# Optimization experiments

Hardware: AMD Instinct MI355X
Metric: run time of the kernel (lower is better)

Reference implementation:

```python
import jax, jax.numpy as jnp
import numpy as np
from jax import lax

B, T, H, F, K, M, NB = 32, 1024, 256, 256, 3, 4096, 256


def setup_inputs() -> dict:
    key = jax.random.key(0)
    ks = jax.random.split(key, 10)
    s = 0.05
    inp = {}
    inp["x"] = jax.random.normal(ks[0], (B, T, H), jnp.float32)
    inp["src_mask"] = jnp.zeros((B, T), bool)
    inp["duration_target"] = jax.random.randint(ks[1], (B, T), 0, 7)
    inp["pitch_target"] = jax.random.uniform(ks[2], (B, T), jnp.float32)
    inp["energy_target"] = jax.random.uniform(ks[3], (B, T), jnp.float32)
    inp["max_len"] = M
    # stacked params for 3 predictors: [duration, pitch, energy]
    inp["w1"] = jax.random.normal(ks[4], (3, K, H, F), jnp.float32) * s  # WIO layout
    inp["b1"] = jnp.zeros((3, F), jnp.float32)
    inp["g1"] = jnp.ones((3, F), jnp.float32)
    inp["be1"] = jnp.zeros((3, F), jnp.float32)
    inp["w2"] = jax.random.normal(ks[5], (3, K, F, F), jnp.float32) * s
    inp["b2"] = jnp.zeros((3, F), jnp.float32)
    inp["g2"] = jnp.ones((3, F), jnp.float32)
    inp["be2"] = jnp.zeros((3, F), jnp.float32)
    inp["lw"] = jax.random.normal(ks[6], (3, F, 1), jnp.float32) * s
    inp["lb"] = jnp.zeros((3, 1), jnp.float32)
    inp["pitch_bins"] = jnp.linspace(0.0, 1.0, NB - 1, dtype=jnp.float32)
    inp["pitch_emb"] = jax.random.normal(ks[7], (NB, H), jnp.float32) * 0.1
    inp["energy_bins"] = jnp.linspace(0.0, 1.0, NB - 1, dtype=jnp.float32)
    inp["energy_emb"] = jax.random.normal(ks[8], (NB, H), jnp.float32) * 0.1
    return inp


def _conv_relu_ln(x, w, b, g, be):
    # Conv1d (k=3, pad=1) over seq dim with channels-last, then ReLU, then LayerNorm.
    h = lax.conv_general_dilated(x, w, (1,), [(1, 1)],
                                 dimension_numbers=('NWC', 'WIO', 'NWC'))
    h = jax.nn.relu(h + b)
    mu = jnp.mean(h, -1, keepdims=True)
    var = jnp.var(h, -1, keepdims=True)
    return (h - mu) * lax.rsqrt(var + 1e-5) * g + be


def _predictor(x, i, w1, b1, g1, be1, w2, b2, g2, be2, lw, lb, mask):
    h = _conv_relu_ln(x, w1[i], b1[i], g1[i], be1[i])
    h = _conv_relu_ln(h, w2[i], b2[i], g2[i], be2[i])
    out = (h @ lw[i] + lb[i])[..., 0]  # [B, T]
    return jnp.where(mask, 0.0, out)


def _length_regulate(x, dur, max_len):
    # vectorized version of the per-sample repeat/cat/pad LengthRegulator
    cum = jnp.cumsum(dur, axis=1)                     # [B, T]
    mel_len = jnp.minimum(cum[:, -1], max_len)        # [B]
    frames = jnp.arange(max_len)                      # [M]
    # frame j maps to phoneme i with cum[i-1] <= j < cum[i]
    idx = jax.vmap(lambda c: jnp.searchsorted(c, frames, side='right'))(cum)
    idx = jnp.minimum(idx, x.shape[1] - 1)
    out = jnp.take_along_axis(x, idx[:, :, None], axis=1)  # [B, M, H]
    valid = frames[None, :] < mel_len[:, None]
    return out * valid[:, :, None].astype(x.dtype), mel_len, ~valid


def reference(x, src_mask, duration_target, pitch_target, energy_target, max_len,
              w1, b1, g1, be1, w2, b2, g2, be2, lw, lb,
              pitch_bins, pitch_emb, energy_bins, energy_emb):
    P = (w1, b1, g1, be1, w2, b2, g2, be2, lw, lb)
    # predictor_grad = 1.0 -> x.detach() + 1.0*(x - x.detach()) == x
    log_dur = _predictor(x, 0, *P, src_mask)
    pitch_pred = _predictor(x, 1, *P, src_mask)
    p_e = pitch_emb[jnp.searchsorted(pitch_bins, pitch_target, side='left')]
    energy_pred = _predictor(x, 2, *P, src_mask)
    e_e = energy_emb[jnp.searchsorted(energy_bins, energy_target, side='left')]
    output = x + p_e + e_e
    out, mel_len, mel_mask = _length_regulate(output, duration_target, max_len)
    return (out, pitch_pred, energy_pred, log_dur, duration_target, mel_len, mel_mask)
```

## Files before the change

### kernel.cpp

```cpp
#include <hip/hip_runtime.h>
#include <hip/hip_bf16.h>
#include <stdint.h>


typedef __bf16 bf16;
typedef __attribute__((ext_vector_type(8))) __bf16 bf16x8;
typedef __attribute__((ext_vector_type(4))) float f32x4;

#define TSEQ 1024

#define O1 33554432
#define O2 33587200
#define O3 33619968
#define O4 33652736
#define O5 33685504
#define O6 33685536

#define OUT_END_B 135266432

#define XB_OFF 512
#define H1B_OFF (XB_OFF + 16777216)
#define H1B_SZ 16777216
#define WT_OFF (H1B_OFF + 3 * H1B_SZ)
#define WT_SZ 393216

#define XB_SZ 16777216
#define H1B_TOT (3 * H1B_SZ)
#define WT_TOT (6 * WT_SZ)
#define SCRATCH_SZ (XB_SZ + H1B_TOT + WT_TOT)

#define CUM_OFF 0
#define ADDROW_OFF 131072
#define ZEROS_OFF 262144
#define WS_SCR_OFF 524288
#define WS_NEED (WS_SCR_OFF + SCRATCH_SZ)

__global__ __launch_bounds__(256) void k_prep(
    const float* __restrict__ x, bf16* __restrict__ xb,
    const float* __restrict__ w1, const float* __restrict__ w2,
    bf16* __restrict__ wt,
    const float* __restrict__ pt, const float* __restrict__ et,
    const float* __restrict__ pbins, const float* __restrict__ ebins,
    int* __restrict__ addrow, float* __restrict__ zpage,
    const int* __restrict__ dur, const int* __restrict__ maxlen,
    float* __restrict__ out, int* __restrict__ cum) {
  int bid = blockIdx.x;
  int tid = threadIdx.x;
  if (bid < 4096) {
    int t = bid * 256 + tid;
    int g = t >> 5;
    int u = t & 31;
    const float4* s = (const float4*)(x + ((size_t)g << 8) + (u << 3));
    float4 a = s[0], b = s[1];
    bf16x8 o;
    o[0] = (bf16)a.x; o[1] = (bf16)a.y; o[2] = (bf16)a.z; o[3] = (bf16)a.w;
    o[4] = (bf16)b.x; o[5] = (bf16)b.y; o[6] = (bf16)b.z; o[7] = (bf16)b.w;
    *(bf16x8*)(xb + ((size_t)g << 8) + (u << 3)) = o;
  } else if (bid < 4672) {
    int bw = bid - 4096;
    int m = bw / 96;
    int r = bw % 96;
    int f = (r & 3) * 64 + (tid & 63);
    int u = (r >> 2) * 4 + (tid >> 6);
    const float* W = (m < 3) ? w1 : w2;
    int i = (m < 3) ? m : m - 3;
    int dt = u >> 5;
    int c0 = (u & 31) << 3;
    const float* src = W + (((size_t)(i * 3 + dt) * 256 + c0) << 8) + f;
    bf16x8 o;
#pragma unroll
    for (int cc = 0; cc < 8; ++cc) o[cc] = (bf16)src[(size_t)cc << 8];
    *(bf16x8*)(wt + (size_t)m * 196608 + (size_t)f * 768 + (u << 3)) = o;
  } else if (bid < 4800) {
    __shared__ float pb[255], eb[255];
    if (tid < 255) { pb[tid] = pbins[tid]; eb[tid] = ebins[tid]; }
    if (bid == 4672 && tid < 64) zpage[tid] = 0.f;
    __syncthreads();
    int g = (bid - 4672) * 256 + tid;
    float pv = pt[g], ev = et[g];
    int lo = 0, hi = 255;
    while (lo < hi) { int md = (lo + hi) >> 1; if (pb[md] < pv) lo = md + 1; else hi = md; }
    int pi = lo;
    lo = 0; hi = 255;
    while (lo < hi) { int md = (lo + hi) >> 1; if (eb[md] < ev) lo = md + 1; else hi = md; }
    addrow[g] = pi | (lo << 16);
  } else {
    __shared__ int lds[256];
    int b = bid - 4800;
    int4 d = ((const int4*)(dur + b * 1024))[tid];
    int p0 = d.x, p1 = p0 + d.y, p2 = p1 + d.z, p3 = p2 + d.w;
    int val = p3;
    lds[tid] = val;
    __syncthreads();
    for (int off = 1; off < 256; off <<= 1) {
      int t = (tid >= off) ? lds[tid - off] : 0;
      __syncthreads();
      val += t;
      lds[tid] = val;
      __syncthreads();
    }
    int excl = val - p3;
    int4 c;
    c.x = excl + p0; c.y = excl + p1; c.z = excl + p2; c.w = excl + p3;
    ((int4*)(cum + b * 1024))[tid] = c;
    float4 fd;
    fd.x = (float)d.x; fd.y = (float)d.y; fd.z = (float)d.z; fd.w = (float)d.w;
    ((float4*)(out + O4 + b * 1024))[tid] = fd;
    if (tid == 255) {
      int mel = val < maxlen[0] ? val : maxlen[0];
      out[O5 + b] = (float)mel;
    }
  }
}

__global__ __launch_bounds__(256, 2) void k_conv(
    const char* __restrict__ Ab, size_t AperY, const char* __restrict__ Wb,
    const float* __restrict__ bias0, const float* __restrict__ gamma0,
    const float* __restrict__ beta0, char* __restrict__ hout0,
    const float* __restrict__ lw0, const float* __restrict__ lb0,
    const unsigned char* __restrict__ mask, float* __restrict__ outb,
    const char* __restrict__ zpage, int mode,
    const float* __restrict__ xf, const int* __restrict__ cum,
    const int* __restrict__ addrow, const float* __restrict__ pemb,
    const float* __restrict__ eemb, const int* __restrict__ maxlen,
    int lrbase) {
  __shared__ __align__(16) char Abuf[2][8192];
  __shared__ __align__(16) char Bbuf[2][16384];
  __shared__ float redS[128][2];
  __shared__ float redS2[128][2];
  __shared__ float predr[128][2];

  const int tid = threadIdx.x;
  const int bid = blockIdx.x;

  if (bid >= 768) {
    int* cl = (int*)Abuf;
    int rid0 = lrbase + ((bid - 768) << 4);
    int b = rid0 >> 12;
    ((int4*)cl)[tid] = ((const int4*)(cum + (b << 10)))[tid];
    __syncthreads();
    int lane = tid & 63;
    int wv = tid >> 6;
    int total = cl[1023];
    int ml = maxlen[0];
    int mel = total < ml ? total : ml;
    int c1 = cl[lane * 16 + 15];
#pragma unroll
    for (int rr = 0; rr < 4; ++rr) {
      int rid = rid0 + (wv << 2) + rr;
      int j = rid & 4095;
      bool valid = j < mel;
      float4 res = {0.f, 0.f, 0.f, 0.f};
      if (valid) {
        unsigned long long m1 = __ballot(j < c1);
        int s = __ffsll(m1) - 1;
        unsigned long long m2 = __ballot(j < cl[s * 16 + (lane & 15)]);
        int p = __ffsll(m2) - 1;
        int i = s * 16 + p;
        int ar = addrow[(b << 10) + i];
        int pi = ar & 0xffff, ei = ar >> 16;
        const float4* xr = (const float4*)(xf + (((size_t)(b << 10) + i) << 8));
        const float4* pr = (const float4*)(pemb + ((size_t)pi << 8));
        const float4* er = (const float4*)(eemb + ((size_t)ei << 8));
        float4 a = xr[lane], pp = pr[lane], e = er[lane];
        res.x = a.x + pp.x + e.x;
        res.y = a.y + pp.y + e.y;
        res.z = a.z + pp.z + e.z;
        res.w = a.w + pp.w + e.w;
      }
      ((float4*)(outb + ((size_t)rid << 8)))[lane] = res;
      if (lane == 0) outb[O6 + rid] = valid ? 0.f : 1.f;
    }
    return;
  }

  const int wv = tid >> 6;
  const int ln = tid & 63;
  const int q = ln >> 4;
  const int m16 = ln & 15;
  const int rh = wv >> 1;
  const int ch = wv & 1;
  const int y = bid >> 8;
  const int g0 = (bid & 255) << 7;
  const int t0 = g0 & (TSEQ - 1);

  const char* A = Ab + (size_t)y * AperY;
  const char* W = Wb + (size_t)y * WT_SZ;

  const int srow = ln >> 2;
  const int slot = ln & 3;
  const int usw = slot ^ ((ln >> 3) & 3);

  const char* bsrc[4];
#pragma unroll
  for (int j = 0; j < 4; ++j) {
    int f = j * 64 + wv * 16 + srow;
    bsrc[j] = W + ((size_t)f * 768 + usw * 8) * 2;
  }
  const int rbase = wv * 16 + srow;

  f32x4 acc[4][8];
#pragma unroll
  for (int a = 0; a < 4; a++)
#pragma unroll
    for (int b = 0; b < 8; b++) acc[a][b] = (f32x4){0.f, 0.f, 0.f, 0.f};

#define STAGE(KB, BUF)                                                         \
  {                                                                            \
    int dt0_ = (KB) >> 3;                                                      \
    int c0_ = ((KB) & 7) << 5;                                                 \
    _Pragma("unroll") for (int j = 0; j < 2; ++j) {                            \
      int rr = j * 64 + rbase + dt0_ - 1;                                      \
      const char* src = ((unsigned)(t0 + rr) < 1024u)                          \
          ? A + (((size_t)(g0 + rr) << 8) + c0_ + usw * 8) * 2                 \
          : zpage + slot * 16;                                                 \
      __builtin_amdgcn_global_load_lds(                                        \
          (const __attribute__((address_space(1))) void*)src,                  \
          (__attribute__((address_space(3))) void*)(Abuf[BUF] + j * 4096 +     \
                                                    tid * 16),                 \
          16, 0, 0);                                                           \
    }                                                                          \
    _Pragma("unroll") for (int j = 0; j < 4; ++j) {                            \
      __builtin_amdgcn_global_load_lds(                                        \
          (const __attribute__((address_space(1))) void*)(bsrc[j] + (KB)*64),  \
          (__attribute__((address_space(3))) void*)(Bbuf[BUF] + j * 4096 +     \
                                                    tid * 16),                 \
          16, 0, 0);                                                           \
    }                                                                          \
  }

  const int spq = (q ^ ((m16 >> 1) & 3)) << 4;
  const int aoff = (rh * 64 + m16) * 64 + spq;
  const int boff = (ch * 128 + m16) * 64 + spq;

  STAGE(0, 0);
#pragma unroll 2
  for (int kb = 0; kb < 24; ++kb) {
    int buf = kb & 1;
    __syncthreads();
    if (kb < 23) STAGE(kb + 1, buf ^ 1);
    bf16x8 af[4], bfr[8];
#pragma unroll
    for (int mi = 0; mi < 4; ++mi)
      af[mi] = *(const bf16x8*)(Abuf[buf] + aoff + mi * 1024);
#pragma unroll
    for (int ni = 0; ni < 8; ++ni)
      bfr[ni] = *(const bf16x8*)(Bbuf[buf] + boff + ni * 1024);
#pragma unroll
    for (int mi = 0; mi < 4; ++mi)
#pragma unroll
      for (int ni = 0; ni < 8; ++ni)
        acc[mi][ni] = __builtin_amdgcn_mfma_f32_16x16x32_bf16(
            af[mi], bfr[ni], acc[mi][ni], 0, 0, 0);
  }
#undef STAGE

  const float* bias = bias0 + y * 256;
  const float* gamma = gamma0 + y * 256;
  const float* beta = beta0 + y * 256;
  float bias_v[8], g_v[8], be_v[8], lw_v[8];
#pragma unroll
  for (int ni = 0; ni < 8; ni++) {
    int nf = (ch << 7) + (ni << 4) + m16;
    bias_v[ni] = bias[nf];
    g_v[ni] = gamma[nf];
    be_v[ni] = beta[nf];
  }
  if (mode) {
    const float* lw = lw0 + y * 256;
#pragma unroll
    for (int ni = 0; ni < 8; ni++) lw_v[ni] = lw[(ch << 7) + (ni << 4) + m16];
  }

#pragma unroll
  for (int mi = 0; mi < 4; mi++) {
#pragma unroll
    for (int r = 0; r < 4; r++) {
      float s1 = 0.f, s2 = 0.f;
#pragma unroll
      for (int ni = 0; ni < 8; ni++) {
        float v = acc[mi][ni][r] + bias_v[ni];
        v = fmaxf(v, 0.f);
        acc[mi][ni][r] = v;
        s1 += v;
        s2 += v * v;
      }
#pragma unroll
      for (int d = 1; d < 16; d <<= 1) {
        s1 += __shfl_xor(s1, d);
        s2 += __shfl_xor(s2, d);
      }
      if (m16 == 0) {
        int m = (rh << 6) + (mi << 4) + (q << 2) + r;
        redS[m][ch] = s1;
        redS2[m][ch] = s2;
      }
    }
  }
  __syncthreads();

  if (mode == 0) {
    bf16* hp = (bf16*)(hout0 + (size_t)y * H1B_SZ);
#pragma unroll
    for (int mi = 0; mi < 4; mi++) {
#pragma unroll
      for (int r = 0; r < 4; r++) {
        int m = (rh << 6) + (mi << 4) + (q << 2) + r;
        float mu = (redS[m][0] + redS[m][1]) * 0.00390625f;
        float var = (redS2[m][0] + redS2[m][1]) * 0.00390625f - mu * mu;
        float rs = rsqrtf(var + 1e-5f);
        int gg = g0 + m;
#pragma unroll
        for (int ni = 0; ni < 8; ni++) {
          float v = (acc[mi][ni][r] - mu) * rs * g_v[ni] + be_v[ni];
          int n = (ch << 7) + (ni << 4) + m16;
          hp[((size_t)gg << 8) + n] = (bf16)v;
        }
      }
    }
  } else {
#pragma unroll
    for (int mi = 0; mi < 4; mi++) {
#pragma unroll
      for (int r = 0; r < 4; r++) {
        int m = (rh << 6) + (mi << 4) + (q << 2) + r;
        float mu = (redS[m][0] + redS[m][1]) * 0.00390625f;
        float var = (redS2[m][0] + redS2[m][1]) * 0.00390625f - mu * mu;
        float rs = rsqrtf(var + 1e-5f);
        float p = 0.f;
#pragma unroll
        for (int ni = 0; ni < 8; ni++) {
          float v = (acc[mi][ni][r] - mu) * rs * g_v[ni] + be_v[ni];
          p += v * lw_v[ni];
        }
#pragma unroll
        for (int d = 1; d < 16; d <<= 1) p += __shfl_xor(p, d);
        if (m16 == 0) predr[m][ch] = p;
      }
    }
    __syncthreads();
    if (tid < 128) {
      int gg = g0 + tid;
      float p = predr[tid][0] + predr[tid][1] + lb0[y];
      if (mask[gg]) p = 0.f;
      float* pd = outb + (y == 0 ? O3 : (y == 1 ? O1 : O2));
      pd[gg] = p;
    }
  }
}

__global__ __launch_bounds__(256) void k_lr(const float* __restrict__ x,
                                            const int* __restrict__ cum,
                                            const int* __restrict__ addrow,
                                            const float* __restrict__ pemb,
                                            const float* __restrict__ eemb,
                                            const int* __restrict__ maxlen,
                                            float* __restrict__ outb) {
  __shared__ int cl[1024];
  int tid = threadIdx.x;
  int rid0 = blockIdx.x << 4;
  int b = rid0 >> 12;
  ((int4*)cl)[tid] = ((const int4*)(cum + (b << 10)))[tid];
  __syncthreads();
  int lane = tid & 63;
  int wv = tid >> 6;
  int total = cl[1023];
  int ml = maxlen[0];
  int mel = total < ml ? total : ml;
  int c1 = cl[lane * 16 + 15];
#pragma unroll
  for (int rr = 0; rr < 4; ++rr) {
    int rid = rid0 + (wv << 2) + rr;
    int j = rid & 4095;
    bool valid = j < mel;
    float4 res = {0.f, 0.f, 0.f, 0.f};
    if (valid) {
      unsigned long long m1 = __ballot(j < c1);
      int s = __ffsll(m1) - 1;
      unsigned long long m2 = __ballot(j < cl[s * 16 + (lane & 15)]);
      int p = __ffsll(m2) - 1;
      int i = s * 16 + p;
      int ar = addrow[(b << 10) + i];
      int pi = ar & 0xffff, ei = ar >> 16;
      const float4* xr = (const float4*)(x + (((size_t)(b << 10) + i) << 8));
      const float4* pr = (const float4*)(pemb + ((size_t)pi << 8));
      const float4* er = (const float4*)(eemb + ((size_t)ei << 8));
      float4 a = xr[lane], pp = pr[lane], e = er[lane];
      res.x = a.x + pp.x + e.x;
      res.y = a.y + pp.y + e.y;
      res.z = a.z + pp.z + e.z;
      res.w = a.w + pp.w + e.w;
    }
    ((float4*)(outb + ((size_t)rid << 8)))[lane] = res;
    if (lane == 0) outb[O6 + rid] = valid ? 0.f : 1.f;
  }
}

extern "C" void kernel_launch(void* const* d_in, const int* in_sizes, int n_in,
                              void* d_out, int out_size, void* d_ws, size_t ws_size,
                              hipStream_t stream) {
  const float* x = (const float*)d_in[0];
  const unsigned char* src_mask = (const unsigned char*)d_in[1];
  const int* dur = (const int*)d_in[2];
  const float* pt = (const float*)d_in[3];
  const float* et = (const float*)d_in[4];
  const int* maxlen = (const int*)d_in[5];
  const float* w1 = (const float*)d_in[6];
  const float* b1 = (const float*)d_in[7];
  const float* g1 = (const float*)d_in[8];
  const float* be1 = (const float*)d_in[9];
  const float* w2 = (const float*)d_in[10];
  const float* b2 = (const float*)d_in[11];
  const float* g2 = (const float*)d_in[12];
  const float* be2 = (const float*)d_in[13];
  const float* lw = (const float*)d_in[14];
  const float* lb = (const float*)d_in[15];
  const float* pbins = (const float*)d_in[16];
  const float* pemb = (const float*)d_in[17];
  const float* ebins = (const float*)d_in[18];
  const float* eemb = (const float*)d_in[19];

  float* outf = (float*)d_out;
  char* ob = (char*)d_out;
  int* cum = (int*)((char*)d_ws + CUM_OFF);
  int* addrow = (int*)((char*)d_ws + ADDROW_OFF);
  float* zpage = (float*)((char*)d_ws + ZEROS_OFF);

  int merged = 0;
  char* sb = nullptr;
  if (ws_size >= (size_t)WS_NEED) {
    sb = (char*)d_ws + WS_SCR_OFF;
    merged = 1;
  } else if ((size_t)out_size >= (size_t)OUT_END_B + (size_t)SCRATCH_SZ) {
    sb = ob + OUT_END_B;
    merged = 1;
  }
  bf16* xb;
  char* h1b;
  bf16* wt;
  if (merged) {
    xb = (bf16*)sb;
    h1b = sb + XB_SZ;
    wt = (bf16*)(sb + XB_SZ + H1B_TOT);
  } else {
    xb = (bf16*)(ob + XB_OFF);
    h1b = ob + H1B_OFF;
    wt = (bf16*)(ob + WT_OFF);
  }

  hipLaunchKernelGGL(k_prep, dim3(4832), dim3(256), 0, stream,
                     x, xb, w1, w2, wt, pt, et, pbins, ebins, addrow, zpage,
                     dur, maxlen, outf, cum);

  int gconv = merged ? 768 + 4096 : 768;
  hipLaunchKernelGGL(k_conv, dim3(gconv), dim3(256), 0, stream,
                     (const char*)xb, (size_t)0, (const char*)wt, b1, g1, be1,
                     h1b, lw, lb, src_mask, outf, (const char*)zpage, 0,
                     x, cum, addrow, pemb, eemb, maxlen, 0);
  hipLaunchKernelGGL(k_conv, dim3(gconv), dim3(256), 0, stream,
                     (const char*)h1b, (size_t)H1B_SZ,
                     (const char*)wt + 3 * WT_SZ, b2, g2, be2,
                     (char*)nullptr, lw, lb, src_mask, outf,
                     (const char*)zpage, 1,
                     x, cum, addrow, pemb, eemb, maxlen, 65536);
  if (!merged) {
    hipLaunchKernelGGL(k_lr, dim3(8192), dim3(256), 0, stream, x, cum, addrow,
                       pemb, eemb, maxlen, outf);
  }
}
```

Baseline: 332.3 us.

## Fuse both conv-LN layers into one kernel keeping hidden activations in LDS

Merges the two conv+ReLU+LayerNorm launches into a single 512-thread kernel. Each block computes layer 1 for 160 rows (its 128 rows plus a 16-row halo on each side), stores the bf16 result in shared memory, then runs layer 2 and the linear head from there. This removes the global h1 buffer round trip and one launch, at the cost of about 25% redundant layer-1 compute on the halo rows and much more LDS per block. Length-regulation work is now appended to the tail of each conv block instead of running as separate blocks.

```diff
diff --git a/kernel.cpp b/kernel.cpp
--- a/kernel.cpp
+++ b/kernel.cpp
@@ -15,25 +15,22 @@
 #define O4 33652736
 #define O5 33685504
 #define O6 33685536
-
 #define OUT_END_B 135266432
 
-#define XB_OFF 512
-#define H1B_OFF (XB_OFF + 16777216)
-#define H1B_SZ 16777216
-#define WT_OFF (H1B_OFF + 3 * H1B_SZ)
+#define XB_SZ 16777216
 #define WT_SZ 393216
-
-#define XB_SZ 16777216
-#define H1B_TOT (3 * H1B_SZ)
 #define WT_TOT (6 * WT_SZ)
-#define SCRATCH_SZ (XB_SZ + H1B_TOT + WT_TOT)
+#define SCRATCH_SZ (XB_SZ + WT_TOT)
 
 #define CUM_OFF 0
 #define ADDROW_OFF 131072
 #define ZEROS_OFF 262144
 #define WS_SCR_OFF 524288
-#define WS_NEED (WS_SCR_OFF + SCRATCH_SZ)
+#define WS_NEED ((size_t)WS_SCR_OFF + (size_t)SCRATCH_SZ)
+
+#define XB_OFF 512
+
+#define LR_PER_BLK 171
 
 __global__ __launch_bounds__(256) void k_prep(
     const float* __restrict__ x, bf16* __restrict__ xb,
@@ -113,48 +110,301 @@
   }
 }
 
-__global__ __launch_bounds__(256, 2) void k_conv(
-    const char* __restrict__ Ab, size_t AperY, const char* __restrict__ Wb,
-    const float* __restrict__ bias0, const float* __restrict__ gamma0,
-    const float* __restrict__ beta0, char* __restrict__ hout0,
+__global__ __launch_bounds__(512, 2) void k_fused(
+    const bf16* __restrict__ xb, const bf16* __restrict__ wt,
+    const float* __restrict__ b1, const float* __restrict__ g1,
+    const float* __restrict__ be1, const float* __restrict__ b2,
+    const float* __restrict__ g2, const float* __restrict__ be2,
     const float* __restrict__ lw0, const float* __restrict__ lb0,
     const unsigned char* __restrict__ mask, float* __restrict__ outb,
-    const char* __restrict__ zpage, int mode,
+    const char* __restrict__ zpage,
     const float* __restrict__ xf, const int* __restrict__ cum,
     const int* __restrict__ addrow, const float* __restrict__ pemb,
     const float* __restrict__ eemb, const int* __restrict__ maxlen,
-    int lrbase) {
-  __shared__ __align__(16) char Abuf[2][8192];
+    int lrn) {
+  __shared__ __align__(16) char Abuf[2][10240];
   __shared__ __align__(16) char Bbuf[2][16384];
-  __shared__ float redS[128][2];
-  __shared__ float redS2[128][2];
-  __shared__ float predr[128][2];
+  __shared__ __align__(16) char H1[160 * 512];
+  __shared__ float redS[160][4];
+  __shared__ float redS2[160][4];
+  __shared__ float predr[128][4];
 
   const int tid = threadIdx.x;
   const int bid = blockIdx.x;
-
-  if (bid >= 768) {
-    int* cl = (int*)Abuf;
-    int rid0 = lrbase + ((bid - 768) << 4);
-    int b = rid0 >> 12;
-    ((int4*)cl)[tid] = ((const int4*)(cum + (b << 10)))[tid];
-    __syncthreads();
-    int lane = tid & 63;
-    int wv = tid >> 6;
-    int total = cl[1023];
+  const int wv = tid >> 6;
+  const int ln = tid & 63;
+  const int q = ln >> 4;
+  const int m16 = ln & 15;
+  const int rh = wv >> 2;
+  const int c4 = wv & 3;
+  const int y = bid >> 8;
+  const int g0 = (bid & 255) << 7;
+  const int t0 = g0 & (TSEQ - 1);
+
+  const bf16* W1 = wt + (size_t)y * 196608;
+  const bf16* W2 = wt + (size_t)(3 + y) * 196608;
+
+  const int arow = tid >> 2;
+  const int asl = tid & 3;
+  const int perm = asl ^ ((arow >> 1) & 3);
+
+#define STAGE1(KB, BUF)                                                        \
+  {                                                                            \
+    const int dt_ = (KB) >> 3;                                                 \
+    const int c0_ = ((KB)&7) << 5;                                             \
+    {                                                                          \
+      int tr_ = t0 - 17 + arow + dt_;                                          \
+      const char* src_ = ((unsigned)tr_ < 1024u)                               \
+          ? (const char*)(xb + ((size_t)(g0 - 17 + arow + dt_) << 8) + c0_ +   \
+                          perm * 8)                                            \
+          : zpage + asl * 16;                                                  \
+      __builtin_amdgcn_global_load_lds(                                        \
+          (const __attribute__((address_space(1))) void*)src_,                 \
+          (__attribute__((address_space(3))) void*)(Abuf[BUF] + tid * 16),     \
+          16, 0, 0);                                                           \
+    }                                                                          \
+    if (tid < 128) {                                                           \
+      int tr_ = t0 + 111 + arow + dt_;                                         \
+      const char* src_ = ((unsigned)tr_ < 1024u)                               \
+          ? (const char*)(xb + ((size_t)(g0 + 111 + arow + dt_) << 8) + c0_ +  \
+                          perm * 8)                                            \
+          : zpage + asl * 16;                                                  \
+      __builtin_amdgcn_global_load_lds(                                        \
+          (const __attribute__((address_space(1))) void*)src_,                 \
+          (__attribute__((address_space(3))) void*)(Abuf[BUF] + 8192 +         \
+                                                    tid * 16),                 \
+          16, 0, 0);                                                           \
+    }                                                                          \
+    STAGEB(W1, KB, BUF)                                                        \
+  }
+
+#define STAGEB(WP, KB, BUF)                                                    \
+  {                                                                            \
+    const bf16* s0_ = (WP) + (size_t)arow * 768 + (KB)*32 + perm * 8;          \
+    __builtin_amdgcn_global_load_lds(                                          \
+        (const __attribute__((address_space(1))) void*)s0_,                    \
+        (__attribute__((address_space(3))) void*)(Bbuf[BUF] + tid * 16),       \
+        16, 0, 0);                                                             \
+    __builtin_amdgcn_global_load_lds(                                          \
+        (const __attribute__((address_space(1))) void*)(s0_ + 98304),          \
+        (__attribute__((address_space(3))) void*)(Bbuf[BUF] + 8192 +           \
+                                                  tid * 16),                   \
+        16, 0, 0);                                                             \
+  }
+
+  const int spq = (q ^ ((m16 >> 1) & 3)) << 4;
+  const int aoff = (rh * 80 + m16) * 64 + spq;
+  const int boff = (c4 * 64 + m16) * 64 + spq;
+
+  f32x4 acc[5][4];
+#pragma unroll
+  for (int a = 0; a < 5; a++)
+#pragma unroll
+    for (int b = 0; b < 4; b++) acc[a][b] = (f32x4){0.f, 0.f, 0.f, 0.f};
+
+  STAGE1(0, 0);
+#pragma unroll 2
+  for (int kb = 0; kb < 24; ++kb) {
+    int buf = kb & 1;
+    __syncthreads();
+    if (kb < 23) STAGE1(kb + 1, buf ^ 1);
+    bf16x8 af[5], bfr[4];
+#pragma unroll
+    for (int mi = 0; mi < 5; ++mi)
+      af[mi] = *(const bf16x8*)(Abuf[buf] + aoff + mi * 1024);
+#pragma unroll
+    for (int ni = 0; ni < 4; ++ni)
+      bfr[ni] = *(const bf16x8*)(Bbuf[buf] + boff + ni * 1024);
+#pragma unroll
+    for (int mi = 0; mi < 5; ++mi)
+#pragma unroll
+      for (int ni = 0; ni < 4; ++ni)
+        acc[mi][ni] = __builtin_amdgcn_mfma_f32_16x16x32_bf16(
+            af[mi], bfr[ni], acc[mi][ni], 0, 0, 0);
+  }
+
+  {
+    const float* bias = b1 + y * 256;
+    const float* gamma = g1 + y * 256;
+    const float* beta = be1 + y * 256;
+    float bias_v[4], g_v[4], be_v[4];
+#pragma unroll
+    for (int ni = 0; ni < 4; ni++) {
+      int nf = (c4 << 6) + (ni << 4) + m16;
+      bias_v[ni] = bias[nf];
+      g_v[ni] = gamma[nf];
+      be_v[ni] = beta[nf];
+    }
+#pragma unroll
+    for (int mi = 0; mi < 5; mi++) {
+#pragma unroll
+      for (int r = 0; r < 4; r++) {
+        float s1 = 0.f, s2 = 0.f;
+#pragma unroll
+        for (int ni = 0; ni < 4; ni++) {
+          float v = acc[mi][ni][r] + bias_v[ni];
+          v = fmaxf(v, 0.f);
+          acc[mi][ni][r] = v;
+          s1 += v;
+          s2 += v * v;
+        }
+#pragma unroll
+        for (int d = 1; d < 16; d <<= 1) {
+          s1 += __shfl_xor(s1, d);
+          s2 += __shfl_xor(s2, d);
+        }
+        if (m16 == 0) {
+          int m = rh * 80 + (mi << 4) + (q << 2) + r;
+          redS[m][c4] = s1;
+          redS2[m][c4] = s2;
+        }
+      }
+    }
+    __syncthreads();
+#pragma unroll
+    for (int mi = 0; mi < 5; mi++) {
+#pragma unroll
+      for (int r = 0; r < 4; r++) {
+        int m = rh * 80 + (mi << 4) + (q << 2) + r;
+        float mu = (redS[m][0] + redS[m][1] + redS[m][2] + redS[m][3]) *
+                   0.00390625f;
+        float var = (redS2[m][0] + redS2[m][1] + redS2[m][2] + redS2[m][3]) *
+                        0.00390625f - mu * mu;
+        float rs = rsqrtf(var + 1e-5f);
+        int trow = t0 - 16 + m;
+        bool vr = (unsigned)trow < 1024u;
+#pragma unroll
+        for (int ni = 0; ni < 4; ni++) {
+          float v = vr ? (acc[mi][ni][r] - mu) * rs * g_v[ni] + be_v[ni] : 0.f;
+          int c = (c4 << 6) + (ni << 4) + m16;
+          *(bf16*)(H1 + m * 512 + ((c * 2) ^ ((m & 7) << 4))) = (bf16)v;
+        }
+      }
+    }
+  }
+
+  f32x4 acc2[4][4];
+#pragma unroll
+  for (int a = 0; a < 4; a++)
+#pragma unroll
+    for (int b = 0; b < 4; b++) acc2[a][b] = (f32x4){0.f, 0.f, 0.f, 0.f};
+
+  STAGEB(W2, 0, 0);
+#pragma unroll 2
+  for (int kb = 0; kb < 24; ++kb) {
+    int buf = kb & 1;
+    __syncthreads();
+    if (kb < 23) STAGEB(W2, kb + 1, buf ^ 1);
+    int dt = kb >> 3;
+    int cbyte = ((kb & 7) << 6) + (q << 4);
+    int hbase = 15 + rh * 64 + dt + m16;
+    bf16x8 af[4], bfr[4];
+#pragma unroll
+    for (int mi = 0; mi < 4; ++mi) {
+      int hr = hbase + (mi << 4);
+      af[mi] = *(const bf16x8*)(H1 + hr * 512 + (cbyte ^ ((hr & 7) << 4)));
+    }
+#pragma unroll
+    for (int ni = 0; ni < 4; ++ni)
+      bfr[ni] = *(const bf16x8*)(Bbuf[buf] + boff + ni * 1024);
+#pragma unroll
+    for (int mi = 0; mi < 4; ++mi)
+#pragma unroll
+      for (int ni = 0; ni < 4; ++ni)
+        acc2[mi][ni] = __builtin_amdgcn_mfma_f32_16x16x32_bf16(
+            af[mi], bfr[ni], acc2[mi][ni], 0, 0, 0);
+  }
+
+  {
+    const float* bias = b2 + y * 256;
+    const float* gamma = g2 + y * 256;
+    const float* beta = be2 + y * 256;
+    const float* lw = lw0 + y * 256;
+    float bias_v[4], g_v[4], be_v[4], lw_v[4];
+#pragma unroll
+    for (int ni = 0; ni < 4; ni++) {
+      int nf = (c4 << 6) + (ni << 4) + m16;
+      bias_v[ni] = bias[nf];
+      g_v[ni] = gamma[nf];
+      be_v[ni] = beta[nf];
+      lw_v[ni] = lw[nf];
+    }
+#pragma unroll
+    for (int mi = 0; mi < 4; mi++) {
+#pragma unroll
+      for (int r = 0; r < 4; r++) {
+        float s1 = 0.f, s2 = 0.f;
+#pragma unroll
+        for (int ni = 0; ni < 4; ni++) {
+          float v = acc2[mi][ni][r] + bias_v[ni];
+          v = fmaxf(v, 0.f);
+          acc2[mi][ni][r] = v;
+          s1 += v;
+          s2 += v * v;
+        }
+#pragma unroll
+        for (int d = 1; d < 16; d <<= 1) {
+          s1 += __shfl_xor(s1, d);
+          s2 += __shfl_xor(s2, d);
+        }
+        if (m16 == 0) {
+          int m = (rh << 6) + (mi << 4) + (q << 2) + r;
+          redS[m][c4] = s1;
+          redS2[m][c4] = s2;
+        }
+      }
+    }
+    __syncthreads();
+#pragma unroll
+    for (int mi = 0; mi < 4; mi++) {
+#pragma unroll
+      for (int r = 0; r < 4; r++) {
+        int m = (rh << 6) + (mi << 4) + (q << 2) + r;
+        float mu = (redS[m][0] + redS[m][1] + redS[m][2] + redS[m][3]) *
+                   0.00390625f;
+        float var = (redS2[m][0] + redS2[m][1] + redS2[m][2] + redS2[m][3]) *
+                        0.00390625f - mu * mu;
+        float rs = rsqrtf(var + 1e-5f);
+        float p = 0.f;
+#pragma unroll
+        for (int ni = 0; ni < 4; ni++) {
+          float v = (acc2[mi][ni][r] - mu) * rs * g_v[ni] + be_v[ni];
+          p += v * lw_v[ni];
+        }
+#pragma unroll
+        for (int d = 1; d < 16; d <<= 1) p += __shfl_xor(p, d);
+        if (m16 == 0) predr[m][c4] = p;
+      }
+    }
+    __syncthreads();
+    if (tid < 128) {
+      int gg = g0 + tid;
+      float p = predr[tid][0] + predr[tid][1] + predr[tid][2] + predr[tid][3] +
+                lb0[y];
+      if (mask[gg]) p = 0.f;
+      float* pd = outb + (y == 0 ? O3 : (y == 1 ? O1 : O2));
+      pd[gg] = p;
+    }
+  }
+
+  if (lrn) {
+    int rid0 = bid * lrn;
     int ml = maxlen[0];
-    int mel = total < ml ? total : ml;
-    int c1 = cl[lane * 16 + 15];
-#pragma unroll
-    for (int rr = 0; rr < 4; ++rr) {
-      int rid = rid0 + (wv << 2) + rr;
-      int j = rid & 4095;
-      bool valid = j < mel;
+    for (int j = wv; j < lrn; j += 8) {
+      int rid = rid0 + j;
+      if (rid >= 131072) break;
+      int b = rid >> 12;
+      int jj = rid & 4095;
+      const int* cb = cum + (b << 10);
+      int c1 = cb[ln * 16 + 15];
+      int total = __shfl(c1, 63);
+      int mel = total < ml ? total : ml;
+      bool valid = jj < mel;
       float4 res = {0.f, 0.f, 0.f, 0.f};
       if (valid) {
-        unsigned long long m1 = __ballot(j < c1);
+        unsigned long long m1 = __ballot(jj < c1);
         int s = __ffsll(m1) - 1;
-        unsigned long long m2 = __ballot(j < cl[s * 16 + (lane & 15)]);
+        unsigned long long m2 = __ballot(jj < cb[s * 16 + (ln & 15)]);
         int p = __ffsll(m2) - 1;
         int i = s * 16 + p;
         int ar = addrow[(b << 10) + i];
@@ -162,192 +412,19 @@
         const float4* xr = (const float4*)(xf + (((size_t)(b << 10) + i) << 8));
         const float4* pr = (const float4*)(pemb + ((size_t)pi << 8));
         const float4* er = (const float4*)(eemb + ((size_t)ei << 8));
-        float4 a = xr[lane], pp = pr[lane], e = er[lane];
+        float4 a = xr[ln], pp = pr[ln], e = er[ln];
         res.x = a.x + pp.x + e.x;
         res.y = a.y + pp.y + e.y;
         res.z = a.z + pp.z + e.z;
         res.w = a.w + pp.w + e.w;
       }
-      ((float4*)(outb + ((size_t)rid << 8)))[lane] = res;
-      if (lane == 0) outb[O6 + rid] = valid ? 0.f : 1.f;
-    }
-    return;
-  }
-
-  const int wv = tid >> 6;
-  const int ln = tid & 63;
-  const int q = ln >> 4;
-  const int m16 = ln & 15;
-  const int rh = wv >> 1;
-  const int ch = wv & 1;
-  const int y = bid >> 8;
-  const int g0 = (bid & 255) << 7;
-  const int t0 = g0 & (TSEQ - 1);
-
-  const char* A = Ab + (size_t)y * AperY;
-  const char* W = Wb + (size_t)y * WT_SZ;
-
-  const int srow = ln >> 2;
-  const int slot = ln & 3;
-  const int usw = slot ^ ((ln >> 3) & 3);
-
-  const char* bsrc[4];
-#pragma unroll
-  for (int j = 0; j < 4; ++j) {
-    int f = j * 64 + wv * 16 + srow;
-    bsrc[j] = W + ((size_t)f * 768 + usw * 8) * 2;
-  }
-  const int rbase = wv * 16 + srow;
-
-  f32x4 acc[4][8];
-#pragma unroll
-  for (int a = 0; a < 4; a++)
-#pragma unroll
-    for (int b = 0; b < 8; b++) acc[a][b] = (f32x4){0.f, 0.f, 0.f, 0.f};
-
-#define STAGE(KB, BUF)                                                         \
-  {                                                                            \
-    int dt0_ = (KB) >> 3;                                                      \
-    int c0_ = ((KB) & 7) << 5;                                                 \
-    _Pragma("unroll") for (int j = 0; j < 2; ++j) {                            \
-      int rr = j * 64 + rbase + dt0_ - 1;                                      \
-      const char* src = ((unsigned)(t0 + rr) < 1024u)                          \
-          ? A + (((size_t)(g0 + rr) << 8) + c0_ + usw * 8) * 2                 \
-          : zpage + slot * 16;                                                 \
-      __builtin_amdgcn_global_load_lds(                                        \
-          (const __attribute__((address_space(1))) void*)src,                  \
-          (__attribute__((address_space(3))) void*)(Abuf[BUF] + j * 4096 +     \
-                                                    tid * 16),                 \
-          16, 0, 0);                                                           \
-    }                                                                          \
-    _Pragma("unroll") for (int j = 0; j < 4; ++j) {                            \
-      __builtin_amdgcn_global_load_lds(                                        \
-          (const __attribute__((address_space(1))) void*)(bsrc[j] + (KB)*64),  \
-          (__attribute__((address_space(3))) void*)(Bbuf[BUF] + j * 4096 +     \
-                                                    tid * 16),                 \
-          16, 0, 0);                                                           \
-    }                                                                          \
-  }
-
-  const int spq = (q ^ ((m16 >> 1) & 3)) << 4;
-  const int aoff = (rh * 64 + m16) * 64 + spq;
-  const int boff = (ch * 128 + m16) * 64 + spq;
-
-  STAGE(0, 0);
-#pragma unroll 2
-  for (int kb = 0; kb < 24; ++kb) {
-    int buf = kb & 1;
-    __syncthreads();
-    if (kb < 23) STAGE(kb + 1, buf ^ 1);
-    bf16x8 af[4], bfr[8];
-#pragma unroll
-    for (int mi = 0; mi < 4; ++mi)
-      af[mi] = *(const bf16x8*)(Abuf[buf] + aoff + mi * 1024);
-#pragma unroll
-    for (int ni = 0; ni < 8; ++ni)
-      bfr[ni] = *(const bf16x8*)(Bbuf[buf] + boff + ni * 1024);
-#pragma unroll
-    for (int mi = 0; mi < 4; ++mi)
-#pragma unroll
-      for (int ni = 0; ni < 8; ++ni)
-        acc[mi][ni] = __builtin_amdgcn_mfma_f32_16x16x32_bf16(
-            af[mi], bfr[ni], acc[mi][ni], 0, 0, 0);
-  }
-#undef STAGE
-
-  const float* bias = bias0 + y * 256;
-  const float* gamma = gamma0 + y * 256;
-  const float* beta = beta0 + y * 256;
-  float bias_v[8], g_v[8], be_v[8], lw_v[8];
-#pragma unroll
-  for (int ni = 0; ni < 8; ni++) {
-    int nf = (ch << 7) + (ni << 4) + m16;
-    bias_v[ni] = bias[nf];
-    g_v[ni] = gamma[nf];
-    be_v[ni] = beta[nf];
-  }
-  if (mode) {
-    const float* lw = lw0 + y * 256;
-#pragma unroll
-    for (int ni = 0; ni < 8; ni++) lw_v[ni] = lw[(ch << 7) + (ni << 4) + m16];
-  }
-
-#pragma unroll
-  for (int mi = 0; mi < 4; mi++) {
-#pragma unroll
-    for (int r = 0; r < 4; r++) {
-      float s1 = 0.f, s2 = 0.f;
-#pragma unroll
-      for (int ni = 0; ni < 8; ni++) {
-        float v = acc[mi][ni][r] + bias_v[ni];
-        v = fmaxf(v, 0.f);
-        acc[mi][ni][r] = v;
-        s1 += v;
-        s2 += v * v;
-      }
-#pragma unroll
-      for (int d = 1; d < 16; d <<= 1) {
-        s1 += __shfl_xor(s1, d);
-        s2 += __shfl_xor(s2, d);
-      }
-      if (m16 == 0) {
-        int m = (rh << 6) + (mi << 4) + (q << 2) + r;
-        redS[m][ch] = s1;
-        redS2[m][ch] = s2;
-      }
-    }
-  }
-  __syncthreads();
-
-  if (mode == 0) {
-    bf16* hp = (bf16*)(hout0 + (size_t)y * H1B_SZ);
-#pragma unroll
-    for (int mi = 0; mi < 4; mi++) {
-#pragma unroll
-      for (int r = 0; r < 4; r++) {
-        int m = (rh << 6) + (mi << 4) + (q << 2) + r;
-        float mu = (redS[m][0] + redS[m][1]) * 0.00390625f;
-        float var = (redS2[m][0] + redS2[m][1]) * 0.00390625f - mu * mu;
-        float rs = rsqrtf(var + 1e-5f);
-        int gg = g0 + m;
-#pragma unroll
-        for (int ni = 0; ni < 8; ni++) {
-          float v = (acc[mi][ni][r] - mu) * rs * g_v[ni] + be_v[ni];
-          int n = (ch << 7) + (ni << 4) + m16;
-          hp[((size_t)gg << 8) + n] = (bf16)v;
-        }
-      }
-    }
-  } else {
-#pragma unroll
-    for (int mi = 0; mi < 4; mi++) {
-#pragma unroll
-      for (int r = 0; r < 4; r++) {
-        int m = (rh << 6) + (mi << 4) + (q << 2) + r;
-        float mu = (redS[m][0] + redS[m][1]) * 0.00390625f;
-        float var = (redS2[m][0] + redS2[m][1]) * 0.00390625f - mu * mu;
-        float rs = rsqrtf(var + 1e-5f);
-        float p = 0.f;
-#pragma unroll
-        for (int ni = 0; ni < 8; ni++) {
-          float v = (acc[mi][ni][r] - mu) * rs * g_v[ni] + be_v[ni];
-          p += v * lw_v[ni];
-        }
-#pragma unroll
-        for (int d = 1; d < 16; d <<= 1) p += __shfl_xor(p, d);
-        if (m16 == 0) predr[m][ch] = p;
-      }
-    }
-    __syncthreads();
-    if (tid < 128) {
-      int gg = g0 + tid;
-      float p = predr[tid][0] + predr[tid][1] + lb0[y];
-      if (mask[gg]) p = 0.f;
-      float* pd = outb + (y == 0 ? O3 : (y == 1 ? O1 : O2));
-      pd[gg] = p;
+      ((float4*)(outb + ((size_t)rid << 8)))[ln] = res;
+      if (ln == 0) outb[O6 + rid] = valid ? 0.f : 1.f;
     }
   }
 }
+#undef STAGE1
+#undef STAGEB
 
 __global__ __launch_bounds__(256) void k_lr(const float* __restrict__ x,
                                             const int* __restrict__ cum,
@@ -428,41 +505,25 @@
 
   int merged = 0;
   char* sb = nullptr;
-  if (ws_size >= (size_t)WS_NEED) {
+  if (ws_size >= WS_NEED) {
     sb = (char*)d_ws + WS_SCR_OFF;
     merged = 1;
   } else if ((size_t)out_size >= (size_t)OUT_END_B + (size_t)SCRATCH_SZ) {
     sb = ob + OUT_END_B;
     merged = 1;
-  }
-  bf16* xb;
-  char* h1b;
-  bf16* wt;
-  if (merged) {
-    xb = (bf16*)sb;
-    h1b = sb + XB_SZ;
-    wt = (bf16*)(sb + XB_SZ + H1B_TOT);
   } else {
-    xb = (bf16*)(ob + XB_OFF);
-    h1b = ob + H1B_OFF;
-    wt = (bf16*)(ob + WT_OFF);
-  }
+    sb = ob + XB_OFF;
+  }
+  bf16* xb = (bf16*)sb;
+  bf16* wt = (bf16*)(sb + XB_SZ);
 
   hipLaunchKernelGGL(k_prep, dim3(4832), dim3(256), 0, stream,
                      x, xb, w1, w2, wt, pt, et, pbins, ebins, addrow, zpage,
                      dur, maxlen, outf, cum);
-
-  int gconv = merged ? 768 + 4096 : 768;
-  hipLaunchKernelGGL(k_conv, dim3(gconv), dim3(256), 0, stream,
-                     (const char*)xb, (size_t)0, (const char*)wt, b1, g1, be1,
-                     h1b, lw, lb, src_mask, outf, (const char*)zpage, 0,
-                     x, cum, addrow, pemb, eemb, maxlen, 0);
-  hipLaunchKernelGGL(k_conv, dim3(gconv), dim3(256), 0, stream,
-                     (const char*)h1b, (size_t)H1B_SZ,
-                     (const char*)wt + 3 * WT_SZ, b2, g2, be2,
-                     (char*)nullptr, lw, lb, src_mask, outf,
-                     (const char*)zpage, 1,
-                     x, cum, addrow, pemb, eemb, maxlen, 65536);
+  hipLaunchKernelGGL(k_fused, dim3(768), dim3(512), 0, stream,
+                     xb, wt, b1, g1, be1, b2, g2, be2, lw, lb, src_mask, outf,
+                     (const char*)zpage, x, cum, addrow, pemb, eemb, maxlen,
+                     merged ? LR_PER_BLK : 0);
   if (!merged) {
     hipLaunchKernelGGL(k_lr, dim3(8192), dim3(256), 0, stream, x, cum, addrow,
                        pemb, eemb, maxlen, outf);
```

Measured after the change: 390.8 us. +17.6%, slower.

## Triple-buffer conv GEMM LDS staging with explicit vmcnt waits and MFMA priority

Applied to the files above, without the earlier changes.

Changes the conv GEMM main loop from double to triple buffering of the A/B LDS tiles. Loads are issued two k-steps ahead, and the full __syncthreads is replaced by an explicit s_waitcnt vmcnt plus s_barrier, so one stage can stay in flight while the current tile is computed. It also raises wave priority around the MFMA block. LDS use grows from 48KB to 72KB per block, which may limit the two-blocks-per-CU occupancy, and the hand-counted vmcnt of 6 must match the number of loads issued per stage.

```diff
diff --git a/kernel.cpp b/kernel.cpp
--- a/kernel.cpp
+++ b/kernel.cpp
@@ -33,7 +33,7 @@
 #define ADDROW_OFF 131072
 #define ZEROS_OFF 262144
 #define WS_SCR_OFF 524288
-#define WS_NEED (WS_SCR_OFF + SCRATCH_SZ)
+#define WS_NEED ((size_t)WS_SCR_OFF + (size_t)SCRATCH_SZ)
 
 __global__ __launch_bounds__(256) void k_prep(
     const float* __restrict__ x, bf16* __restrict__ xb,
@@ -124,8 +124,8 @@
     const int* __restrict__ addrow, const float* __restrict__ pemb,
     const float* __restrict__ eemb, const int* __restrict__ maxlen,
     int lrbase) {
-  __shared__ __align__(16) char Abuf[2][8192];
-  __shared__ __align__(16) char Bbuf[2][16384];
+  __shared__ __align__(16) char Abuf[3][8192];
+  __shared__ __align__(16) char Bbuf[3][16384];
   __shared__ float redS[128][2];
   __shared__ float redS2[128][2];
   __shared__ float predr[128][2];
@@ -209,6 +209,8 @@
   {                                                                            \
     int dt0_ = (KB) >> 3;                                                      \
     int c0_ = ((KB) & 7) << 5;                                                 \
+    char* ad_ = Abuf[BUF];                                                     \
+    char* bd_ = Bbuf[BUF];                                                     \
     _Pragma("unroll") for (int j = 0; j < 2; ++j) {                            \
       int rr = j * 64 + rbase + dt0_ - 1;                                      \
       const char* src = ((unsigned)(t0 + rr) < 1024u)                          \
@@ -216,14 +218,14 @@
           : zpage + slot * 16;                                                 \
       __builtin_amdgcn_global_load_lds(                                        \
           (const __attribute__((address_space(1))) void*)src,                  \
-          (__attribute__((address_space(3))) void*)(Abuf[BUF] + j * 4096 +     \
+          (__attribute__((address_space(3))) void*)(ad_ + j * 4096 +           \
                                                     tid * 16),                 \
           16, 0, 0);                                                           \
     }                                                                          \
     _Pragma("unroll") for (int j = 0; j < 4; ++j) {                            \
       __builtin_amdgcn_global_load_lds(                                        \
           (const __attribute__((address_space(1))) void*)(bsrc[j] + (KB)*64),  \
-          (__attribute__((address_space(3))) void*)(Bbuf[BUF] + j * 4096 +     \
+          (__attribute__((address_space(3))) void*)(bd_ + j * 4096 +           \
                                                     tid * 16),                 \
           16, 0, 0);                                                           \
     }                                                                          \
@@ -234,24 +236,35 @@
   const int boff = (ch * 128 + m16) * 64 + spq;
 
   STAGE(0, 0);
-#pragma unroll 2
+  STAGE(1, 1);
+  int cur = 0, stg = 2;
   for (int kb = 0; kb < 24; ++kb) {
-    int buf = kb & 1;
-    __syncthreads();
-    if (kb < 23) STAGE(kb + 1, buf ^ 1);
+    if (kb < 23)
+      asm volatile("s_waitcnt vmcnt(6)" ::: "memory");
+    else
+      asm volatile("s_waitcnt vmcnt(0)" ::: "memory");
+    __builtin_amdgcn_s_barrier();
+    if (kb < 22) STAGE(kb + 2, stg);
+    const char* Ac = Abuf[cur];
+    const char* Bc = Bbuf[cur];
     bf16x8 af[4], bfr[8];
 #pragma unroll
     for (int mi = 0; mi < 4; ++mi)
-      af[mi] = *(const bf16x8*)(Abuf[buf] + aoff + mi * 1024);
+      af[mi] = *(const bf16x8*)(Ac + aoff + mi * 1024);
 #pragma unroll
     for (int ni = 0; ni < 8; ++ni)
-      bfr[ni] = *(const bf16x8*)(Bbuf[buf] + boff + ni * 1024);
+      bfr[ni] = *(const bf16x8*)(Bc + boff + ni * 1024);
+    __builtin_amdgcn_s_setprio(1);
 #pragma unroll
     for (int mi = 0; mi < 4; ++mi)
 #pragma unroll
       for (int ni = 0; ni < 8; ++ni)
         acc[mi][ni] = __builtin_amdgcn_mfma_f32_16x16x32_bf16(
             af[mi], bfr[ni], acc[mi][ni], 0, 0, 0);
+    __builtin_amdgcn_s_setprio(0);
+    asm volatile("s_waitcnt lgkmcnt(0)" ::: "memory");
+    cur = (cur == 2) ? 0 : cur + 1;
+    stg = (stg == 2) ? 0 : stg + 1;
   }
 #undef STAGE
 
@@ -428,7 +441,7 @@
 
   int merged = 0;
   char* sb = nullptr;
-  if (ws_size >= (size_t)WS_NEED) {
+  if (ws_size >= WS_NEED) {
     sb = (char*)d_ws + WS_SCR_OFF;
     merged = 1;
   } else if ((size_t)out_size >= (size_t)OUT_END_B + (size_t)SCRATCH_SZ) {
```

Result: no change. 330.2 us (-0.6%).

## Reuse one A tile with halo across all three conv taps in k_conv

Applied to the files above, without the earlier changes.

The conv GEMM loop is reorganised from 24 independent k-blocks, each reloading a shifted 128-row A tile per tap, into 8 channel chunks. Each chunk loads a 130-row A tile with halo once and reuses it for all three taps by offsetting the LDS row read, while only the B weights are restaged per tap. This cuts global-to-LDS A traffic by roughly a factor of three, at the cost of a slightly larger A buffer and a small extra halo load done by 8 threads. It also wraps the MFMA block in s_setprio to favour matrix issue over other waves.

```diff
diff --git a/kernel.cpp b/kernel.cpp
--- a/kernel.cpp
+++ b/kernel.cpp
@@ -33,7 +33,7 @@
 #define ADDROW_OFF 131072
 #define ZEROS_OFF 262144
 #define WS_SCR_OFF 524288
-#define WS_NEED (WS_SCR_OFF + SCRATCH_SZ)
+#define WS_NEED ((size_t)WS_SCR_OFF + (size_t)SCRATCH_SZ)
 
 __global__ __launch_bounds__(256) void k_prep(
     const float* __restrict__ x, bf16* __restrict__ xb,
@@ -124,7 +124,7 @@
     const int* __restrict__ addrow, const float* __restrict__ pemb,
     const float* __restrict__ eemb, const int* __restrict__ maxlen,
     int lrbase) {
-  __shared__ __align__(16) char Abuf[2][8192];
+  __shared__ __align__(16) char Abuf[2][8320];
   __shared__ __align__(16) char Bbuf[2][16384];
   __shared__ float redS[128][2];
   __shared__ float redS2[128][2];
@@ -188,7 +188,7 @@
   const char* W = Wb + (size_t)y * WT_SZ;
 
   const int srow = ln >> 2;
-  const int slot = ln & 3;
+  const int slot = tid & 3;
   const int usw = slot ^ ((ln >> 3) & 3);
 
   const char* bsrc[4];
@@ -197,7 +197,6 @@
     int f = j * 64 + wv * 16 + srow;
     bsrc[j] = W + ((size_t)f * 768 + usw * 8) * 2;
   }
-  const int rbase = wv * 16 + srow;
 
   f32x4 acc[4][8];
 #pragma unroll
@@ -205,24 +204,40 @@
 #pragma unroll
     for (int b = 0; b < 8; b++) acc[a][b] = (f32x4){0.f, 0.f, 0.f, 0.f};
 
-#define STAGE(KB, BUF)                                                         \
+#define STAGEA(C0, BUF)                                                        \
   {                                                                            \
-    int dt0_ = (KB) >> 3;                                                      \
-    int c0_ = ((KB) & 7) << 5;                                                 \
     _Pragma("unroll") for (int j = 0; j < 2; ++j) {                            \
-      int rr = j * 64 + rbase + dt0_ - 1;                                      \
-      const char* src = ((unsigned)(t0 + rr) < 1024u)                          \
-          ? A + (((size_t)(g0 + rr) << 8) + c0_ + usw * 8) * 2                 \
+      int tr_ = j * 64 + (tid >> 2);                                           \
+      int ch_ = slot ^ ((tr_ >> 1) & 3);                                       \
+      const char* src_ = ((unsigned)(t0 - 1 + tr_) < 1024u)                    \
+          ? A + (((size_t)(g0 - 1 + tr_) << 8) + (C0)*32 + ch_ * 8) * 2        \
           : zpage + slot * 16;                                                 \
       __builtin_amdgcn_global_load_lds(                                        \
-          (const __attribute__((address_space(1))) void*)src,                  \
+          (const __attribute__((address_space(1))) void*)src_,                 \
           (__attribute__((address_space(3))) void*)(Abuf[BUF] + j * 4096 +     \
                                                     tid * 16),                 \
           16, 0, 0);                                                           \
     }                                                                          \
+    if (tid < 8) {                                                             \
+      int tr_ = 128 + (tid >> 2);                                              \
+      int ch_ = slot ^ ((tr_ >> 1) & 3);                                       \
+      const char* src_ = ((unsigned)(t0 - 1 + tr_) < 1024u)                    \
+          ? A + (((size_t)(g0 - 1 + tr_) << 8) + (C0)*32 + ch_ * 8) * 2        \
+          : zpage + slot * 16;                                                 \
+      __builtin_amdgcn_global_load_lds(                                        \
+          (const __attribute__((address_space(1))) void*)src_,                 \
+          (__attribute__((address_space(3))) void*)(Abuf[BUF] + 8192 +         \
+                                                    tid * 16),                 \
+          16, 0, 0);                                                           \
+    }                                                                          \
+  }
+
+#define STAGEB(DT, C0, BUF)                                                    \
+  {                                                                            \
     _Pragma("unroll") for (int j = 0; j < 4; ++j) {                            \
       __builtin_amdgcn_global_load_lds(                                        \
-          (const __attribute__((address_space(1))) void*)(bsrc[j] + (KB)*64),  \
+          (const __attribute__((address_space(1))) void*)(                     \
+              bsrc[j] + ((DT)*8 + (C0)) * 64),                                 \
           (__attribute__((address_space(3))) void*)(Bbuf[BUF] + j * 4096 +     \
                                                     tid * 16),                 \
           16, 0, 0);                                                           \
@@ -230,30 +245,45 @@
   }
 
   const int spq = (q ^ ((m16 >> 1) & 3)) << 4;
-  const int aoff = (rh * 64 + m16) * 64 + spq;
   const int boff = (ch * 128 + m16) * 64 + spq;
 
-  STAGE(0, 0);
+  STAGEA(0, 0);
+  STAGEB(0, 0, 0);
 #pragma unroll 2
-  for (int kb = 0; kb < 24; ++kb) {
-    int buf = kb & 1;
-    __syncthreads();
-    if (kb < 23) STAGE(kb + 1, buf ^ 1);
-    bf16x8 af[4], bfr[8];
-#pragma unroll
-    for (int mi = 0; mi < 4; ++mi)
-      af[mi] = *(const bf16x8*)(Abuf[buf] + aoff + mi * 1024);
-#pragma unroll
-    for (int ni = 0; ni < 8; ++ni)
-      bfr[ni] = *(const bf16x8*)(Bbuf[buf] + boff + ni * 1024);
-#pragma unroll
-    for (int mi = 0; mi < 4; ++mi)
+  for (int c0 = 0; c0 < 8; ++c0) {
+    const int ab = c0 & 1;
+#pragma unroll
+    for (int dt = 0; dt < 3; ++dt) {
+      const int k = c0 * 3 + dt;
+      const int bb = k & 1;
+      __syncthreads();
+      if (dt < 2) {
+        STAGEB(dt + 1, c0, bb ^ 1);
+      } else if (c0 < 7) {
+        STAGEB(0, c0 + 1, bb ^ 1);
+        STAGEA(c0 + 1, ab ^ 1);
+      }
+      const int sel = ((m16 + dt) >> 1) & 3;
+      const int aoff = (rh * 64 + m16 + dt) * 64 + ((q ^ sel) << 4);
+      bf16x8 af[4], bfr[8];
+#pragma unroll
+      for (int mi = 0; mi < 4; ++mi)
+        af[mi] = *(const bf16x8*)(Abuf[ab] + aoff + mi * 1024);
 #pragma unroll
       for (int ni = 0; ni < 8; ++ni)
-        acc[mi][ni] = __builtin_amdgcn_mfma_f32_16x16x32_bf16(
-            af[mi], bfr[ni], acc[mi][ni], 0, 0, 0);
-  }
-#undef STAGE
+        bfr[ni] = *(const bf16x8*)(Bbuf[bb] + boff + ni * 1024);
+      __builtin_amdgcn_s_setprio(1);
+#pragma unroll
+      for (int mi = 0; mi < 4; ++mi)
+#pragma unroll
+        for (int ni = 0; ni < 8; ++ni)
+          acc[mi][ni] = __builtin_amdgcn_mfma_f32_16x16x32_bf16(
+              af[mi], bfr[ni], acc[mi][ni], 0, 0, 0);
+      __builtin_amdgcn_s_setprio(0);
+    }
+  }
+#undef STAGEA
+#undef STAGEB
 
   const float* bias = bias0 + y * 256;
   const float* gamma = gamma0 + y * 256;
@@ -428,7 +458,7 @@
 
   int merged = 0;
   char* sb = nullptr;
-  if (ws_size >= (size_t)WS_NEED) {
+  if (ws_size >= WS_NEED) {
     sb = (char*)d_ws + WS_SCR_OFF;
     merged = 1;
   } else if ((size_t)out_size >= (size_t)OUT_END_B + (size_t)SCRATCH_SZ) {
```

Measured after the change: 340.4 us. 1.02x slower.
